# Kernel tuning notes

Hardware: AMD Instinct MI355X
Metric: run time of the kernel (lower is better)

Reference implementation:

```python
import jax, jax.numpy as jnp
import numpy as np

KH, KW = 3, 3
PAD = 1
C_IN, C_OUT = 64, 128


def unfold(x, kh, kw, pad):
    # x: (B, C, H, W) -> (B, C, kh*kw, H*W), torch.nn.functional.unfold ordering
    B, C, H, W = x.shape
    xp = jnp.pad(x, ((0, 0), (0, 0), (pad, pad), (pad, pad)))
    patches = jnp.stack(
        [xp[:, :, i:i + H, j:j + W] for i in range(kh) for j in range(kw)],
        axis=2,
    )  # (B, C, K, H, W)
    return patches.reshape(B, C, kh * kw, H * W)


def setup_inputs() -> dict:
    key = jax.random.key(0)
    k1, k2, k3 = jax.random.split(key, 3)
    B, H, W = 8, 128, 128
    inp = jax.random.normal(k1, (B, C_IN, H, W), dtype=jnp.float32)
    g_buffer = jax.random.uniform(k2, (B, 2, H, W), dtype=jnp.float32)
    # weights param as in torch: (1, C*kh*kw, 1, out_channels), kaiming-uniform-ish
    wdepth = C_IN * KH * KW
    bound = float(np.sqrt(6.0 / wdepth))
    weights = jax.random.uniform(k3, (1, wdepth, 1, C_OUT), dtype=jnp.float32,
                                 minval=-bound, maxval=bound)
    bias = jnp.zeros((C_OUT,), dtype=jnp.float32)
    return {"input": inp, "g_buffer": g_buffer, "weights": weights, "bias": bias}


def reference(input, g_buffer, weights, bias):
    B, C, H, W = input.shape
    K = KH * KW
    L = H * W
    depth = 2.0 * (g_buffer[:, -1:, :, :] - 0.5)  # (B, 1, H, W)

    input_unf = unfold(input, KH, KW, PAD)          # (B, C, K, L)
    depth_unf = unfold(depth, KH, KW, PAD)          # (B, 1, K, L)

    # bilateral depth weighting
    dfeat = depth_unf - depth.reshape(B, 1, 1, L)   # (B, 1, K, L)
    dfeat = jnp.sum(dfeat * dfeat, axis=1)          # (B, K, L)
    wf = jnp.exp(-dfeat)
    wf = 9.0 * wf / jnp.sum(wf, axis=1, keepdims=True)  # (B, K, L)

    filt = input_unf * wf[:, None, :, :]            # (B, C, K, L)
    filt = filt.reshape(B, C * K, L)

    W2 = weights.reshape(C_OUT, C * K)              # raw reshape, matches torch .view
    out_unf = jnp.einsum('bkl,ok->bol', filt, W2)   # (B, C_OUT, L)
    out = out_unf.reshape(B, C_OUT, H, W) + bias[None, :, None, None]
    return out
```

## Files before the change

### kernel.cpp

```cpp
#include <hip/hip_runtime.h>
#include <hip/hip_bf16.h>
#include <stdint.h>

typedef _Float16 f16x8 __attribute__((ext_vector_type(8)));
typedef float    f32x4 __attribute__((ext_vector_type(4)));

#define CIN   64
#define COUT  128
#define HH    128
#define WW    128
#define BB    8

#define TROW  130
#define ROWBYTES (130 * 128)
#define TSIZE ((size_t)BB * TROW * ROWBYTES)

#define AS1 __attribute__((address_space(1)))
#define AS3 __attribute__((address_space(3)))


__global__ void prep_plus(const float* __restrict__ wflat, _Float16* __restrict__ bp,
                          _Float16* __restrict__ T) {
    int gid = blockIdx.x * 256 + threadIdx.x;
    if (gid < 8 * 18 * 64 * 8) {
        int j = gid & 7;
        int l = (gid >> 3) & 63;
        int s = (gid >> 9) % 18;
        int n = gid / (18 * 512);
        int o = n * 16 + (l & 15);
        int c = ((s & 1) << 5) + ((l >> 4) << 3) + j;
        int k = s >> 1;
        bp[gid] = (_Float16)wflat[o * 576 + c * 9 + k];
        return;
    }
    int h = gid - 8 * 18 * 64 * 8;
    if (h < 16 * 1040) {
        int row = h / 1040, c = h - row * 1040;
        int b = row >> 1, yp = (row & 1) * 129;
        f16x8 z = {};
        *(f16x8*)((char*)T + (size_t)(b * TROW + yp) * ROWBYTES + c * 16) = z;
    }
}

__global__ __launch_bounds__(256) void transpose_pass(const float* __restrict__ inp,
                                                      _Float16* __restrict__ T) {
    __shared__ float sT[64][129];
    const int b   = blockIdx.x >> 7;
    const int y   = blockIdx.x & 127;
    const int tid = threadIdx.x;

    const float* ib = inp + ((long)b * CIN * HH + y) * WW;
    const int xq = tid & 31, c8 = tid >> 5;
    #pragma unroll
    for (int i = 0; i < 8; ++i) {
        int c = c8 * 8 + i;
        float4 v = *(const float4*)(ib + (long)c * (HH * WW) + (xq << 2));
        *(float4*)&sT[c][xq << 2] = v;
    }
    __syncthreads();

    const int x  = tid & 127;
    const int ch = tid >> 7;
    char* rowp = (char*)T + (size_t)(b * TROW + y + 1) * ROWBYTES + (size_t)(x + 1) * 128;
    const int sw = (x + 1) & 7;
    for (int c0 = ch * 8; c0 < 64; c0 += 16) {
        f16x8 v;
        #pragma unroll
        for (int j = 0; j < 8; ++j) v[j] = (_Float16)sT[c0 + j][x];
        *(f16x8*)(rowp + (((c0 >> 3) ^ sw) << 4)) = v;
    }
    if (tid < 16) {
        char* basep = (char*)T + (size_t)(b * TROW + y + 1) * ROWBYTES
                    + ((tid >> 3) ? 129 * 128 : 0) + (tid & 7) * 16;
        f16x8 z = {};
        *(f16x8*)basep = z;
    }
}

__global__ __launch_bounds__(256, 2) void depthcnn_main(
    const _Float16* __restrict__ T, const float* __restrict__ gbuf,
    const float* __restrict__ bias, const _Float16* __restrict__ aprep,
    float* __restrict__ out)
{
    __shared__ __align__(1024) char sIn[4 * ROWBYTES];
    __shared__ _Float16 sWf[2][9][128];

    const int blk    = blockIdx.x;
    const int b      = blk & 7;
    const int strip  = blk >> 3;
    const int ystart = strip << 1;

    const int tid  = threadIdx.x;
    const int wave = tid >> 6;
    const int lane = tid & 63;
    const int l15  = lane & 15;
    const int g4   = lane >> 4;
    const int x0w  = wave << 5;

    {
        const char* Tb = (const char*)T + ((size_t)b * TROW + ystart) * ROWBYTES;
        #pragma unroll
        for (int tt = 0; tt < 17; ++tt) {
            int t = tt * 256 + tid;
            if (t < 4 * 1040) {
                int tr = t / 1040, c = t - tr * 1040;
                __builtin_amdgcn_global_load_lds(
                    (const AS1 uint32_t*)(Tb + (size_t)tr * ROWBYTES + c * 16),
                    (AS3 uint32_t*)(sIn + tr * ROWBYTES + c * 16), 16, 0, 0);
            }
        }
    }

    const char* ap = (const char*)aprep + lane * 16;
    f16x8 af[2][8];
    #pragma unroll
    for (int ot = 0; ot < 8; ++ot)
        af[0][ot] = *(const f16x8*)(ap + (size_t)(ot * 18) * 1024);

    {
        const int r = tid >> 7, px = tid & 127, y = ystart + r;
        const float* g = gbuf + ((size_t)b * 2 + 1) * (HH * WW);
        float dc = 2.f * (g[y * WW + px] - 0.5f);
        float e[9];
        float ssum = 0.f;
        #pragma unroll
        for (int k = 0; k < 9; ++k) {
            int yy = y + (k / 3) - 1;
            int xx = px + (k % 3) - 1;
            float dn = 0.f;
            if ((unsigned)yy < 128u && (unsigned)xx < 128u)
                dn = 2.f * (g[yy * WW + xx] - 0.5f);
            float df = dn - dc;
            float ek = __expf(-df * df);
            e[k] = ek;
            ssum += ek;
        }
        float sc = 9.f / ssum;
        #pragma unroll
        for (int k = 0; k < 9; ++k) sWf[r][k][px] = (_Float16)(e[k] * sc);
    }

    __syncthreads();

    const char* binA[3][2];
    #pragma unroll
    for (int d = 0; d < 3; ++d)
        #pragma unroll
        for (int ch = 0; ch < 2; ++ch)
            binA[d][ch] = sIn + (x0w << 7) + (((l15 + d) << 7)
                        + ((((ch << 2) | g4) ^ ((l15 + d) & 7)) << 4));
    const char* bwf = (const char*)&sWf[0][0][0] + ((x0w + l15) << 1);

    f32x4 acc[2][2][8];
    #pragma unroll
    for (int r = 0; r < 2; ++r)
        #pragma unroll
        for (int pt = 0; pt < 2; ++pt)
            #pragma unroll
            for (int ot = 0; ot < 8; ++ot)
                acc[r][pt][ot] = (f32x4){0.f, 0.f, 0.f, 0.f};

    #pragma unroll
    for (int s = 0; s < 18; ++s) {
        if (s < 17) {
            #pragma unroll
            for (int ot = 0; ot < 8; ++ot)
                af[(s + 1) & 1][ot] = *(const f16x8*)(ap + (size_t)(ot * 18 + s + 1) * 1024);
        }
        const int tap = s >> 1;
        const int ch  = s & 1;
        const int dy  = tap / 3;
        const int dx  = tap - 3 * dy;
        #pragma unroll
        for (int r = 0; r < 2; ++r) {
            _Float16 wh[2];
            #pragma unroll
            for (int pt = 0; pt < 2; ++pt)
                wh[pt] = *(const _Float16*)(bwf + ((r * 9 + tap) * 256 + pt * 32));
            f16x8 bf[2];
            #pragma unroll
            for (int pt = 0; pt < 2; ++pt) {
                f16x8 iv = *(const f16x8*)(binA[dx][ch]
                         + ((r + dy) * ROWBYTES + (pt << 11)));
                f16x8 w8 = {wh[pt], wh[pt], wh[pt], wh[pt],
                            wh[pt], wh[pt], wh[pt], wh[pt]};
                bf[pt] = iv * w8;
            }
            __builtin_amdgcn_s_setprio(1);
            #pragma unroll
            for (int ot = 0; ot < 8; ++ot) {
                acc[r][0][ot] = __builtin_amdgcn_mfma_f32_16x16x32_f16(
                    af[s & 1][ot], bf[0], acc[r][0][ot], 0, 0, 0);
                acc[r][1][ot] = __builtin_amdgcn_mfma_f32_16x16x32_f16(
                    af[s & 1][ot], bf[1], acc[r][1][ot], 0, 0, 0);
            }
            __builtin_amdgcn_s_setprio(0);
        }
    }

    float* ob = out + (size_t)b * COUT * (HH * WW);
    #pragma unroll
    for (int ot = 0; ot < 8; ++ot) {
        #pragma unroll
        for (int r4 = 0; r4 < 4; ++r4) {
            const int o = (ot << 4) + (g4 << 2) + r4;
            const float bv = bias[o];
            #pragma unroll
            for (int r = 0; r < 2; ++r) {
                #pragma unroll
                for (int pt = 0; pt < 2; ++pt) {
                    const int px = x0w + (pt << 4) + l15;
                    ob[(size_t)o * (HH * WW) + (size_t)(ystart + r) * WW + px]
                        = acc[r][pt][ot][r4] + bv;
                }
            }
        }
    }
}

extern "C" void kernel_launch(void* const* d_in, const int* in_sizes, int n_in,
                              void* d_out, int out_size, void* d_ws, size_t ws_size,
                              hipStream_t stream) {
    const float* inp  = (const float*)d_in[0];
    const float* gbuf = (const float*)d_in[1];
    const float* wts  = (const float*)d_in[2];
    const float* bias = (const float*)d_in[3];

    _Float16* T  = (_Float16*)d_ws;
    _Float16* bp = (_Float16*)((char*)d_ws + TSIZE);

    hipLaunchKernelGGL(prep_plus, dim3(353), dim3(256), 0, stream, wts, bp, T);
    hipLaunchKernelGGL(transpose_pass, dim3(BB * HH), dim3(256), 0, stream, inp, T);
    hipLaunchKernelGGL(depthcnn_main, dim3(512), dim3(256), 0, stream,
                       T, gbuf, bias, bp, (float*)d_out);
}
```

Before: 47.58 us.

## Process one output row per block in main conv kernel for more blocks

The main kernel now computes one output row per block instead of two, so it launches 1024 blocks, loads 3 halo rows into LDS instead of 4, halves the accumulator registers and raises launch bounds to allow three blocks per CU. The aim is more occupancy and parallelism, at the cost of more halo re-reading (3 rows per output row instead of 2) and reloading the weight fragments twice as often. The transpose pass also reorders its block index so batch varies fastest, and the depth weights are now computed by half of each wave.

Result: slower. 68.43 us (+43.8%).

```diff
diff --git a/kernel.cpp b/kernel.cpp
--- a/kernel.cpp
+++ b/kernel.cpp
@@ -45,8 +45,8 @@
 __global__ __launch_bounds__(256) void transpose_pass(const float* __restrict__ inp,
                                                       _Float16* __restrict__ T) {
     __shared__ float sT[64][129];
-    const int b   = blockIdx.x >> 7;
-    const int y   = blockIdx.x & 127;
+    const int b   = blockIdx.x & 7;
+    const int y   = blockIdx.x >> 3;
     const int tid = threadIdx.x;
 
     const float* ib = inp + ((long)b * CIN * HH + y) * WW;
@@ -77,18 +77,17 @@
     }
 }
 
-__global__ __launch_bounds__(256, 2) void depthcnn_main(
+__global__ __launch_bounds__(256, 3) void depthcnn_main(
     const _Float16* __restrict__ T, const float* __restrict__ gbuf,
     const float* __restrict__ bias, const _Float16* __restrict__ aprep,
     float* __restrict__ out)
 {
-    __shared__ __align__(1024) char sIn[4 * ROWBYTES];
-    __shared__ _Float16 sWf[2][9][128];
-
-    const int blk    = blockIdx.x;
-    const int b      = blk & 7;
-    const int strip  = blk >> 3;
-    const int ystart = strip << 1;
+    __shared__ __align__(1024) char sIn[3 * ROWBYTES];
+    __shared__ _Float16 sWf[9][128];
+
+    const int blk = blockIdx.x;
+    const int b   = blk & 7;
+    const int y   = blk >> 3;
 
     const int tid  = threadIdx.x;
     const int wave = tid >> 6;
@@ -98,16 +97,12 @@
     const int x0w  = wave << 5;
 
     {
-        const char* Tb = (const char*)T + ((size_t)b * TROW + ystart) * ROWBYTES;
-        #pragma unroll
-        for (int tt = 0; tt < 17; ++tt) {
-            int t = tt * 256 + tid;
-            if (t < 4 * 1040) {
-                int tr = t / 1040, c = t - tr * 1040;
-                __builtin_amdgcn_global_load_lds(
-                    (const AS1 uint32_t*)(Tb + (size_t)tr * ROWBYTES + c * 16),
-                    (AS3 uint32_t*)(sIn + tr * ROWBYTES + c * 16), 16, 0, 0);
-            }
+        const char* Tb = (const char*)T + ((size_t)b * TROW + y) * ROWBYTES;
+        for (int t = tid; t < 3 * 1040; t += 256) {
+            int tr = t / 1040, c = t - tr * 1040;
+            __builtin_amdgcn_global_load_lds(
+                (const AS1 uint32_t*)(Tb + (size_t)tr * ROWBYTES + c * 16),
+                (AS3 uint32_t*)(sIn + tr * ROWBYTES + c * 16), 16, 0, 0);
         }
     }
 
@@ -117,8 +112,8 @@
     for (int ot = 0; ot < 8; ++ot)
         af[0][ot] = *(const f16x8*)(ap + (size_t)(ot * 18) * 1024);
 
-    {
-        const int r = tid >> 7, px = tid & 127, y = ystart + r;
+    if ((lane & 63) < 32) {
+        const int px = (wave << 5) | lane;
         const float* g = gbuf + ((size_t)b * 2 + 1) * (HH * WW);
         float dc = 2.f * (g[y * WW + px] - 0.5f);
         float e[9];
@@ -137,7 +132,7 @@
         }
         float sc = 9.f / ssum;
         #pragma unroll
-        for (int k = 0; k < 9; ++k) sWf[r][k][px] = (_Float16)(e[k] * sc);
+        for (int k = 0; k < 9; ++k) sWf[k][px] = (_Float16)(e[k] * sc);
     }
 
     __syncthreads();
@@ -146,19 +141,19 @@
     #pragma unroll
     for (int d = 0; d < 3; ++d)
         #pragma unroll
-        for (int ch = 0; ch < 2; ++ch)
-            binA[d][ch] = sIn + (x0w << 7) + (((l15 + d) << 7)
-                        + ((((ch << 2) | g4) ^ ((l15 + d) & 7)) << 4));
-    const char* bwf = (const char*)&sWf[0][0][0] + ((x0w + l15) << 1);
-
-    f32x4 acc[2][2][8];
-    #pragma unroll
-    for (int r = 0; r < 2; ++r)
-        #pragma unroll
-        for (int pt = 0; pt < 2; ++pt)
-            #pragma unroll
-            for (int ot = 0; ot < 8; ++ot)
-                acc[r][pt][ot] = (f32x4){0.f, 0.f, 0.f, 0.f};
+        for (int ch = 0; ch < 2; ++ch) {
+            const int xp = x0w + l15 + d;
+            binA[d][ch] = sIn + ((xp << 7)
+                        + ((((ch << 2) | g4) ^ (xp & 7)) << 4));
+        }
+    const char* bwf = (const char*)&sWf[0][0] + ((x0w + l15) << 1);
+
+    f32x4 acc[2][8];
+    #pragma unroll
+    for (int pt = 0; pt < 2; ++pt)
+        #pragma unroll
+        for (int ot = 0; ot < 8; ++ot)
+            acc[pt][ot] = (f32x4){0.f, 0.f, 0.f, 0.f};
 
     #pragma unroll
     for (int s = 0; s < 18; ++s) {
@@ -171,34 +166,31 @@
         const int ch  = s & 1;
         const int dy  = tap / 3;
         const int dx  = tap - 3 * dy;
-        #pragma unroll
-        for (int r = 0; r < 2; ++r) {
-            _Float16 wh[2];
-            #pragma unroll
-            for (int pt = 0; pt < 2; ++pt)
-                wh[pt] = *(const _Float16*)(bwf + ((r * 9 + tap) * 256 + pt * 32));
-            f16x8 bf[2];
-            #pragma unroll
-            for (int pt = 0; pt < 2; ++pt) {
-                f16x8 iv = *(const f16x8*)(binA[dx][ch]
-                         + ((r + dy) * ROWBYTES + (pt << 11)));
-                f16x8 w8 = {wh[pt], wh[pt], wh[pt], wh[pt],
-                            wh[pt], wh[pt], wh[pt], wh[pt]};
-                bf[pt] = iv * w8;
-            }
-            __builtin_amdgcn_s_setprio(1);
-            #pragma unroll
-            for (int ot = 0; ot < 8; ++ot) {
-                acc[r][0][ot] = __builtin_amdgcn_mfma_f32_16x16x32_f16(
-                    af[s & 1][ot], bf[0], acc[r][0][ot], 0, 0, 0);
-                acc[r][1][ot] = __builtin_amdgcn_mfma_f32_16x16x32_f16(
-                    af[s & 1][ot], bf[1], acc[r][1][ot], 0, 0, 0);
-            }
-            __builtin_amdgcn_s_setprio(0);
-        }
-    }
-
-    float* ob = out + (size_t)b * COUT * (HH * WW);
+
+        _Float16 wh[2];
+        #pragma unroll
+        for (int pt = 0; pt < 2; ++pt)
+            wh[pt] = *(const _Float16*)(bwf + (tap * 256 + pt * 32));
+        f16x8 bf[2];
+        #pragma unroll
+        for (int pt = 0; pt < 2; ++pt) {
+            f16x8 iv = *(const f16x8*)(binA[dx][ch] + (dy * ROWBYTES + (pt << 11)));
+            f16x8 w8 = {wh[pt], wh[pt], wh[pt], wh[pt],
+                        wh[pt], wh[pt], wh[pt], wh[pt]};
+            bf[pt] = iv * w8;
+        }
+        __builtin_amdgcn_s_setprio(1);
+        #pragma unroll
+        for (int ot = 0; ot < 8; ++ot) {
+            acc[0][ot] = __builtin_amdgcn_mfma_f32_16x16x32_f16(
+                af[s & 1][ot], bf[0], acc[0][ot], 0, 0, 0);
+            acc[1][ot] = __builtin_amdgcn_mfma_f32_16x16x32_f16(
+                af[s & 1][ot], bf[1], acc[1][ot], 0, 0, 0);
+        }
+        __builtin_amdgcn_s_setprio(0);
+    }
+
+    float* ob = out + (size_t)b * COUT * (HH * WW) + (size_t)y * WW;
     #pragma unroll
     for (int ot = 0; ot < 8; ++ot) {
         #pragma unroll
@@ -206,13 +198,9 @@
             const int o = (ot << 4) + (g4 << 2) + r4;
             const float bv = bias[o];
             #pragma unroll
-            for (int r = 0; r < 2; ++r) {
-                #pragma unroll
-                for (int pt = 0; pt < 2; ++pt) {
-                    const int px = x0w + (pt << 4) + l15;
-                    ob[(size_t)o * (HH * WW) + (size_t)(ystart + r) * WW + px]
-                        = acc[r][pt][ot][r4] + bv;
-                }
+            for (int pt = 0; pt < 2; ++pt) {
+                const int px = x0w + (pt << 4) + l15;
+                ob[(size_t)o * (HH * WW) + px] = acc[pt][ot][r4] + bv;
             }
         }
     }
@@ -231,6 +219,6 @@
 
     hipLaunchKernelGGL(prep_plus, dim3(353), dim3(256), 0, stream, wts, bp, T);
     hipLaunchKernelGGL(transpose_pass, dim3(BB * HH), dim3(256), 0, stream, inp, T);
-    hipLaunchKernelGGL(depthcnn_main, dim3(512), dim3(256), 0, stream,
+    hipLaunchKernelGGL(depthcnn_main, dim3(BB * HH), dim3(256), 0, stream,
                        T, gbuf, bias, bp, (float*)d_out);
 }
```
